# Optimization experiments

Hardware: AMD Instinct MI355X
Metric: run time of the kernel (lower is better)

Reference implementation:

```python
import jax, jax.numpy as jnp
import numpy as np

T, S, B, H, NH, F = 256, 128, 32, 1024, 16, 4096
D = H // NH  # head dim


def setup_inputs() -> dict:
    key = jax.random.key(0)
    ks = jax.random.split(key, 14)
    w = lambda k, shape: jax.random.normal(k, shape, jnp.float32) * 0.02
    return {
        "x": jax.random.normal(ks[0], (T, B, H), jnp.float32),
        "src_bias": jnp.zeros((B, 1, 1, S), jnp.float32),
        "tgt_bias": jnp.zeros((B, 1, 1, T), jnp.float32),
        "memory": jax.random.normal(ks[1], (S, B, H), jnp.float32),
        # cross-attention projections
        "Wq": w(ks[2], (H, H)), "bq": jnp.zeros((H,), jnp.float32),
        "Wk": w(ks[3], (H, H)), "bk": jnp.zeros((H,), jnp.float32),
        "Wv": w(ks[4], (H, H)), "bv": jnp.zeros((H,), jnp.float32),
        "Wo": w(ks[5], (H, H)), "bo": jnp.zeros((H,), jnp.float32),
        # feed-forward
        "W1": w(ks[6], (H, F)), "b1": jnp.zeros((F,), jnp.float32),
        "W2": w(ks[7], (F, H)), "b2": jnp.zeros((H,), jnp.float32),
        # LSTM gates: input = cat(ffn_x, attn_ctx, h) -> 3H, output 4H (i,j,f,o)
        "Wg": w(ks[8], (3 * H, 4 * H)), "bg": jnp.zeros((4 * H,), jnp.float32),
    }


def _cross_attention(xq, mem, bias, Wq, bq, Wk, bk, Wv, bv, Wo, bo):
    # xq: [B,T,H], mem: [B,S,H], bias: [B,1,1,S]
    b, t, h = xq.shape
    q = (xq @ Wq + bq).reshape(b, t, NH, D) * (D ** -0.5)
    k = (mem @ Wk + bk).reshape(b, -1, NH, D)
    v = (mem @ Wv + bv).reshape(b, -1, NH, D)
    logits = jnp.einsum("bqhd,bkhd->bhqk", q, k) + bias
    wts = jax.nn.softmax(logits, axis=-1)
    ctx = jnp.einsum("bhqk,bkhd->bqhd", wts, v).reshape(b, t, h)
    return ctx @ Wo + bo


def reference(x, src_bias, tgt_bias, memory, Wq, bq, Wk, bk, Wv, bv, Wo, bo,
              W1, b1, W2, b2, Wg, bg):
    # cross attention (time-major -> batch-major -> time-major)
    c_attn = _cross_attention(jnp.transpose(x, (1, 0, 2)),
                              jnp.transpose(memory, (1, 0, 2)),
                              src_bias, Wq, bq, Wk, bk, Wv, bv, Wo, bo)
    c_attn = jnp.transpose(c_attn, (1, 0, 2))  # [T,B,H]

    # feed-forward on x (dropout disabled / eval mode)
    ffn_x = jax.nn.relu(x @ W1 + b1) @ W2 + b2  # [T,B,H]

    xs = jnp.concatenate([ffn_x, c_attn], axis=-1)  # [T,B,2H]
    c0 = jnp.zeros((x.shape[1], H), x.dtype)
    h0 = jnp.zeros((x.shape[1], H), x.dtype)

    def step(carry, xt):
        c, h = carry
        g = jnp.concatenate([xt, h], axis=-1) @ Wg + bg  # [B,4H]
        i = jax.nn.sigmoid(g[:, :H])
        j = jnp.tanh(g[:, H:2 * H])
        f = jax.nn.sigmoid(g[:, 2 * H:3 * H])
        o = jax.nn.sigmoid(g[:, 3 * H:])
        new_c = f * c + i * j
        new_h = o * new_c  # THUMT LSTMCell default activation=None
        return (new_c, new_h), new_h

    (c_f, h_f), hiddens = jax.lax.scan(step, (c0, h0), xs)
    return hiddens, c_f, h_f
```

## Files before the change

### kernel.cpp

```cpp
#include <hip/hip_runtime.h>
#include <cstdint>
#include <cstddef>

#define T_  256
#define S_  128
#define B_  32
#define H_  1024
#define NH_ 16
#define D_  64
#define F_  4096
#define TB_ (T_*B_)
#define SB_ (S_*B_)

typedef unsigned short u16;
typedef unsigned int   u32;
typedef unsigned long long u64;
typedef __attribute__((ext_vector_type(8))) short s16x8;
typedef __attribute__((ext_vector_type(4))) float f32x4;
typedef __attribute__((ext_vector_type(4))) u32  u32x4;

static __device__ __forceinline__ float b2f(u16 u) {
  union { u32 i; float f; } cv; cv.i = ((u32)u) << 16; return cv.f;
}
static __device__ __forceinline__ u16 f2b(float f) {
  union { float f; u32 i; } cv; cv.f = f;
  u32 u = cv.i;
  u32 r = (u + 0x7fffu + ((u >> 16) & 1u)) >> 16;
  return (u16)r;
}
static __device__ __forceinline__ float sigm(float x) {
  return 1.0f / (1.0f + __expf(-x));
}
static __device__ __forceinline__ float tanh_fast(float x) {
  float e2 = __expf(2.0f * x);
  return 1.0f - 2.0f / (e2 + 1.0f);
}

typedef const __attribute__((address_space(1))) void* gvoidp;
typedef __attribute__((address_space(3))) void* lvoidp;
static __device__ __forceinline__ void gl_lds16(const void* g, void* l) {
  __builtin_amdgcn_global_load_lds((gvoidp)g, (lvoidp)l, 16, 0, 0);
}

static __device__ __forceinline__ void cast_task(const float* __restrict__ in,
                                                 u16* __restrict__ out, int lb, int tid) {
  int i = lb * 256 + tid;
  float4 v = reinterpret_cast<const float4*>(in)[i];
  ushort4 o;
  o.x = f2b(v.x); o.y = f2b(v.y); o.z = f2b(v.z); o.w = f2b(v.w);
  reinterpret_cast<ushort4*>(out)[i] = o;
}

static __device__ __forceinline__ void tr32(const float* __restrict__ in,
                                            u16* __restrict__ out,
                                            int R, int C, int lin, int tid,
                                            float tile[32][33]) {
  const int gx = C >> 5;
  const int bx = lin % gx, by = lin / gx;
  const int c0 = bx << 5, r0 = by << 5;
  const int tx = tid & 31, ty = tid >> 5;
  #pragma unroll
  for (int k = 0; k < 32; k += 8)
    tile[ty + k][tx] = in[(size_t)(r0 + ty + k) * C + c0 + tx];
  __syncthreads();
  #pragma unroll
  for (int k = 0; k < 32; k += 8)
    out[(size_t)(c0 + ty + k) * R + r0 + tx] = f2b(tile[tx][ty + k]);
}

#define NB_SENT 1
#define NB_CX   8192
#define NB_CM   4096
#define NB_TSQ  1024
#define NB_TW1  4096
#define NB_TW2  4096
#define NB_TGX  8192
#define NB_TWH  4096
#define NB_PREP (NB_SENT + NB_CX + NB_CM + 4*NB_TSQ + NB_TW1 + NB_TW2 + NB_TGX + NB_TWH)

__global__ __launch_bounds__(256) void prep_all(
    const float* __restrict__ x, const float* __restrict__ mem,
    const float* __restrict__ Wq, const float* __restrict__ Wk,
    const float* __restrict__ Wv, const float* __restrict__ Wo,
    const float* __restrict__ W1, const float* __restrict__ W2,
    const float* __restrict__ Wg,
    u16* __restrict__ xb, u16* __restrict__ memb,
    u16* __restrict__ WqT, u16* __restrict__ WkT, u16* __restrict__ WvT,
    u16* __restrict__ WoT, u16* __restrict__ W1T, u16* __restrict__ W2T,
    u16* __restrict__ WgxT, u16* __restrict__ WhT, u32* __restrict__ sent)
{
  __shared__ float tile[32][33];
  int b = blockIdx.x;
  const int tid = threadIdx.x;
  if (b < NB_SENT) { sent[tid] = 0; sent[tid + 256] = 0; return; }
  b -= NB_SENT;
  if (b < NB_CX) { cast_task(x, xb, b, tid); return; }      b -= NB_CX;
  if (b < NB_CM) { cast_task(mem, memb, b, tid); return; }  b -= NB_CM;
  if (b < NB_TSQ) { tr32(Wq, WqT, H_, H_, b, tid, tile); return; }  b -= NB_TSQ;
  if (b < NB_TSQ) { tr32(Wk, WkT, H_, H_, b, tid, tile); return; }  b -= NB_TSQ;
  if (b < NB_TSQ) { tr32(Wv, WvT, H_, H_, b, tid, tile); return; }  b -= NB_TSQ;
  if (b < NB_TSQ) { tr32(Wo, WoT, H_, H_, b, tid, tile); return; }  b -= NB_TSQ;
  if (b < NB_TW1) { tr32(W1, W1T, H_, F_, b, tid, tile); return; }  b -= NB_TW1;
  if (b < NB_TW2) { tr32(W2, W2T, F_, H_, b, tid, tile); return; }  b -= NB_TW2;
  if (b < NB_TGX) { tr32(Wg, WgxT, 2 * H_, 4 * H_, b, tid, tile); return; } b -= NB_TGX;
  tr32(Wg + (size_t)(2 * H_) * (4 * H_), WhT, H_, 4 * H_, b, tid, tile);
}

#define SBAR      asm volatile("s_barrier" ::: "memory")
#define VMCNT4    asm volatile("s_waitcnt vmcnt(4)" ::: "memory")
#define VMCNT0    asm volatile("s_waitcnt vmcnt(0)" ::: "memory")

struct GJob {
  const u16* A; const u16* Bt; u16* Out; const float* bias;
  int Kdim; int ostride; int relu; int gridx; int nblk; float scale;
};
struct GBatch { GJob j[4]; int starts[4]; int njobs; };

static __device__ __forceinline__ void stage_region(
    const u16* __restrict__ src, int Kdim, int row0,
    int kt, int kh, char* lds_region, int tid) {
  const int w  = tid >> 6;
  const int r  = tid >> 2;
  const int cs = (tid & 3) ^ ((tid >> 3) & 3);
  const int kbase = kt * 64 + kh * 32 + cs * 8;
  gl_lds16(src + (size_t)(row0 + r) * Kdim + kbase,        lds_region + w * 1024);
  gl_lds16(src + (size_t)(row0 + 128 + r) * Kdim + kbase,  lds_region + 8192 + w * 1024);
}

static __device__ __forceinline__ s16x8 ldsf(const char* sm, int base, int row, int quad) {
  return *(const s16x8*)(sm + base + row * 64 + ((quad ^ ((row >> 1) & 3)) << 4));
}

__global__ __launch_bounds__(512, 2) void gemm256(GBatch gb)
{
  __shared__ __align__(16) u16 smem[65536];
  char* sm = (char*)smem;
  const int bid = blockIdx.x;
  int ji = 0;
  #pragma unroll
  for (int t = 1; t < 4; t++)
    if (t < gb.njobs && bid >= gb.starts[t]) ji = t;
  const GJob J = gb.j[ji];
  const int lin = bid - gb.starts[ji];
  const int wg = (lin & 7) * (J.nblk >> 3) + (lin >> 3);
  const int bx = wg % J.gridx, by = wg / J.gridx;
  const int bm = by << 8, bn = bx << 8;

  const int tid = threadIdx.x;
  const int wavei = tid >> 6, lane = tid & 63;
  const int quad = lane >> 4, l16 = lane & 15;
  const int wm = wavei >> 2, wn = wavei & 3;
  const int NT = J.Kdim >> 6;
  const int arow = wm * 128;
  const int brow = wn * 64;

  f32x4 acc[8][4] = {};

  stage_region(J.A,  J.Kdim, bm, 0, 0, sm + 0,     tid);
  stage_region(J.Bt, J.Kdim, bn, 0, 0, sm + 32768, tid);
  stage_region(J.A,  J.Kdim, bm, 0, 1, sm + 16384, tid);
  stage_region(J.Bt, J.Kdim, bn, 0, 1, sm + 49152, tid);
  VMCNT4;
  SBAR;

  for (int kt = 0; kt < NT; kt++) {
    const int p = (kt & 1) << 16;
    const int q = p ^ 65536;
    const int Ab = p, Bb = p + 32768;
    const bool st = (kt + 1 < NT);
    s16x8 af[8], b0, b1;

    #pragma unroll
    for (int mi = 0; mi < 8; mi++)
      af[mi] = ldsf(sm, Ab, arow + mi * 16 + l16, quad);
    b0 = ldsf(sm, Bb, brow + l16, quad);
    b1 = ldsf(sm, Bb, brow + 16 + l16, quad);
    if (st) stage_region(J.A, J.Kdim, bm, kt + 1, 0, sm + q, tid);
    SBAR;
    __builtin_amdgcn_s_setprio(1);
    #pragma unroll
    for (int mi = 0; mi < 8; mi++) {
      acc[mi][0] = __builtin_amdgcn_mfma_f32_16x16x32_bf16(af[mi], b0, acc[mi][0], 0, 0, 0);
      acc[mi][1] = __builtin_amdgcn_mfma_f32_16x16x32_bf16(af[mi], b1, acc[mi][1], 0, 0, 0);
    }
    __builtin_amdgcn_s_setprio(0);
    SBAR;

    b0 = ldsf(sm, Bb, brow + 32 + l16, quad);
    b1 = ldsf(sm, Bb, brow + 48 + l16, quad);
    if (st) stage_region(J.Bt, J.Kdim, bn, kt + 1, 0, sm + q + 32768, tid);
    SBAR;
    __builtin_amdgcn_s_setprio(1);
    #pragma unroll
    for (int mi = 0; mi < 8; mi++) {
      acc[mi][2] = __builtin_amdgcn_mfma_f32_16x16x32_bf16(af[mi], b0, acc[mi][2], 0, 0, 0);
      acc[mi][3] = __builtin_amdgcn_mfma_f32_16x16x32_bf16(af[mi], b1, acc[mi][3], 0, 0, 0);
    }
    __builtin_amdgcn_s_setprio(0);
    if (st) { VMCNT4; } else { VMCNT0; }
    SBAR;

    const int Ab1 = Ab + 16384, Bb1 = Bb + 16384;
    #pragma unroll
    for (int mi = 0; mi < 8; mi++)
      af[mi] = ldsf(sm, Ab1, arow + mi * 16 + l16, quad);
    b0 = ldsf(sm, Bb1, brow + l16, quad);
    b1 = ldsf(sm, Bb1, brow + 16 + l16, quad);
    if (st) stage_region(J.A, J.Kdim, bm, kt + 1, 1, sm + q + 16384, tid);
    SBAR;
    __builtin_amdgcn_s_setprio(1);
    #pragma unroll
    for (int mi = 0; mi < 8; mi++) {
      acc[mi][0] = __builtin_amdgcn_mfma_f32_16x16x32_bf16(af[mi], b0, acc[mi][0], 0, 0, 0);
      acc[mi][1] = __builtin_amdgcn_mfma_f32_16x16x32_bf16(af[mi], b1, acc[mi][1], 0, 0, 0);
    }
    __builtin_amdgcn_s_setprio(0);
    SBAR;

    b0 = ldsf(sm, Bb1, brow + 32 + l16, quad);
    b1 = ldsf(sm, Bb1, brow + 48 + l16, quad);
    if (st) stage_region(J.Bt, J.Kdim, bn, kt + 1, 1, sm + q + 49152, tid);
    SBAR;
    __builtin_amdgcn_s_setprio(1);
    #pragma unroll
    for (int mi = 0; mi < 8; mi++) {
      acc[mi][2] = __builtin_amdgcn_mfma_f32_16x16x32_bf16(af[mi], b0, acc[mi][2], 0, 0, 0);
      acc[mi][3] = __builtin_amdgcn_mfma_f32_16x16x32_bf16(af[mi], b1, acc[mi][3], 0, 0, 0);
    }
    __builtin_amdgcn_s_setprio(0);
    if (st) { VMCNT4; }
    SBAR;
  }

  #pragma unroll
  for (int mi = 0; mi < 8; mi++) {
    #pragma unroll
    for (int nj = 0; nj < 4; nj++) {
      const int colo = bn + wn * 64 + nj * 16 + l16;
      const float bv = J.bias[colo];
      #pragma unroll
      for (int r = 0; r < 4; r++) {
        const int rowo = bm + wm * 128 + mi * 16 + quad * 4 + r;
        float vv = (acc[mi][nj][r] + bv) * J.scale;
        if (J.relu) vv = fmaxf(vv, 0.0f);
        J.Out[(size_t)rowo * J.ostride + colo] = f2b(vv);
      }
    }
  }
}

__global__ __launch_bounds__(256) void attn_kernel(
    const u16* __restrict__ q, const u16* __restrict__ k, const u16* __restrict__ v,
    const float* __restrict__ src_bias, u16* __restrict__ ctx)
{
  __shared__ u16 ks[S_ * D_];
  __shared__ u16 vs[S_ * D_];
  const int b  = blockIdx.x >> 4;
  const int nh = blockIdx.x & 15;
  const int tid = threadIdx.x;

  for (int i = tid; i < (S_ * D_) / 8; i += 256) {
    int s = i >> 3, c = (i & 7) * 8;
    *(uint4*)&ks[s * D_ + c] = *(const uint4*)&k[((size_t)(s * B_ + b)) * H_ + nh * D_ + c];
    *(uint4*)&vs[s * D_ + c] = *(const uint4*)&v[((size_t)(s * B_ + b)) * H_ + nh * D_ + c];
  }
  __syncthreads();

  const int t = tid;
  float qf[D_];
  const u16* qp = &q[((size_t)(t * B_ + b)) * H_ + nh * D_];
  #pragma unroll
  for (int c8 = 0; c8 < D_; c8 += 8) {
    uint4 qv = *(const uint4*)&qp[c8];
    const u16* pu = (const u16*)&qv;
    #pragma unroll
    for (int j = 0; j < 8; j++) qf[c8 + j] = b2f(pu[j]);
  }
  const float* bias = src_bias + b * S_;

  float m = -1e30f, l = 0.0f;
  for (int s = 0; s < S_; s++) {
    float dot = 0.0f;
    #pragma unroll
    for (int d = 0; d < D_; d++) dot += qf[d] * b2f(ks[s * D_ + d]);
    dot += bias[s];
    float nm = fmaxf(m, dot);
    l = l * __expf(m - nm) + __expf(dot - nm);
    m = nm;
  }
  float of[D_] = {};
  const float inv = 1.0f / l;
  for (int s = 0; s < S_; s++) {
    float dot = 0.0f;
    #pragma unroll
    for (int d = 0; d < D_; d++) dot += qf[d] * b2f(ks[s * D_ + d]);
    dot += bias[s];
    float w = __expf(dot - m) * inv;
    #pragma unroll
    for (int d = 0; d < D_; d++) of[d] += w * b2f(vs[s * D_ + d]);
  }
  u16* op = &ctx[((size_t)(t * B_ + b)) * H_ + nh * D_];
  #pragma unroll
  for (int c8 = 0; c8 < D_; c8 += 8) {
    u16 tmp[8];
    #pragma unroll
    for (int j = 0; j < 8; j++) tmp[j] = f2b(of[c8 + j]);
    *(uint4*)&op[c8] = *(const uint4*)tmp;
  }
}

#define ISSUE2(K) { \
  const u16* b0_ = hb + ((size_t)(wave * 16 + (K) * 2 + (quad >> 1))) * 512 + \
                   (quad & 1) * 8 + l16 * 16; \
  asm volatile("global_load_dwordx4 %0, %1, off sc0 sc1" : "=v"(ba[K][0]) : "v"(b0_) : "memory"); \
  asm volatile("global_load_dwordx4 %0, %1, off sc0 sc1" : "=v"(ba[K][1]) : "v"(b0_ + 256) : "memory"); }

#define DO_MFMA(A0,A1,KC)                                                           \
  { _Pragma("unroll") for (int g_ = 0; g_ < 3; g_++) {                              \
      s16x8 wf_ = *(const s16x8*)&Wl[wave][((g_ * 8 + (KC)) * 64 + lane) * 8];      \
      acc[g_][0] = __builtin_amdgcn_mfma_f32_16x16x32_bf16(A0, wf_, acc[g_][0], 0, 0, 0); \
      acc[g_][1] = __builtin_amdgcn_mfma_f32_16x16x32_bf16(A1, wf_, acc[g_][1], 0, 0, 0); } \
    acc[3][0] = __builtin_amdgcn_mfma_f32_16x16x32_bf16(A0, wo[KC], acc[3][0], 0, 0, 0);  \
    acc[3][1] = __builtin_amdgcn_mfma_f32_16x16x32_bf16(A1, wo[KC], acc[3][1], 0, 0, 0); }

#define CONSUME(K, NSTR) { \
  asm volatile("s_waitcnt vmcnt(" NSTR ")" ::: "memory"); \
  __builtin_amdgcn_sched_barrier(0); \
  DO_MFMA(ba[K][0], ba[K][1], K); }

__global__ __launch_bounds__(256, 1) void lstm_persistent(
    const u16* __restrict__ g_x, const u16* __restrict__ WhT,
    u16* __restrict__ hb16, u32* __restrict__ sent, float* __restrict__ out)
{
  __shared__ __align__(16) u16 Wl[4][3 * 8 * 64 * 8];
  __shared__ float P[4][4][32][17];
  const int bk = blockIdx.x, tid = threadIdx.x;
  const int wave = tid >> 6, lane = tid & 63;
  const int quad = lane >> 4, l16 = lane & 15;

  for (int i = lane; i < 3 * 8 * 64; i += 64) {
    const int g  = (i >> 9) & 3;
    const int kc = (i >> 6) & 7;
    const int row = g * H_ + bk * 16 + (lane & 15);
    const int col = wave * 256 + kc * 32 + (lane >> 4) * 8;
    *(uint4*)&Wl[wave][i * 8] = *(const uint4*)&WhT[(size_t)row * H_ + col];
  }
  s16x8 wo[8];
  {
    const int row = 3 * H_ + bk * 16 + (lane & 15);
    const int colb = wave * 256 + (lane >> 4) * 8;
    #pragma unroll
    for (int kc = 0; kc < 8; kc++)
      wo[kc] = *(const s16x8*)&WhT[(size_t)row * H_ + colb + kc * 32];
  }
  __syncthreads();

  const int pb = tid >> 4, pc = tid & 15;
  const int col = bk * 16 + pc;
  float creg[2] = {0.0f, 0.0f};

  float gxp[2][4];
  #pragma unroll
  for (int ii = 0; ii < 2; ii++)
    #pragma unroll
    for (int g = 0; g < 4; g++)
      gxp[ii][g] = b2f(g_x[((size_t)(pb + ii * 16)) * (4 * H_) + g * H_ + col]);

  s16x8 ba[8][2];

  for (int t = 0; t < T_; t++) {
    if (t > 0) {
      const u32 st = (u32)t;
      const u16* hb = hb16 + ((t & 1) ^ 1) * 32768;

      { const u32* sp = sent + ((size_t)(((t & 1) ^ 1) * 256 + wave * 64 + lane));
        u32 sv;
        do {
          asm volatile("global_load_dword %0, %1, off sc0 sc1\n\ts_waitcnt vmcnt(0)"
                       : "=v"(sv) : "v"(sp) : "memory");
        } while (!__all(sv == st)); }

      f32x4 acc[4][2] = {};
      ISSUE2(0) ISSUE2(1) ISSUE2(2) ISSUE2(3)
      ISSUE2(4) ISSUE2(5) ISSUE2(6) ISSUE2(7)
      CONSUME(0, "14") CONSUME(1, "12") CONSUME(2, "10") CONSUME(3, "8")
      CONSUME(4, "6")  CONSUME(5, "4")  CONSUME(6, "2")  CONSUME(7, "0")

      #pragma unroll
      for (int g = 0; g < 4; g++)
        #pragma unroll
        for (int mt = 0; mt < 2; mt++)
          #pragma unroll
          for (int r = 0; r < 4; r++)
            P[wave][g][mt * 16 + quad * 4 + r][l16] = acc[g][mt][r];
    }
    __syncthreads();

    float gs[2][4];
    #pragma unroll
    for (int ii = 0; ii < 2; ii++) {
      const int b_ = pb + ii * 16;
      #pragma unroll
      for (int g = 0; g < 4; g++) {
        float s = gxp[ii][g];
        if (t > 0) s += P[0][g][b_][pc] + P[1][g][b_][pc] + P[2][g][b_][pc] + P[3][g][b_][pc];
        gs[ii][g] = s;
      }
    }
    __syncthreads();

    float hn[2], cn[2];
    #pragma unroll
    for (int ii = 0; ii < 2; ii++) {
      const float iv = sigm(gs[ii][0]);
      const float jv = tanh_fast(gs[ii][1]);
      const float fv = sigm(gs[ii][2]);
      const float ov = sigm(gs[ii][3]);
      cn[ii] = fv * creg[ii] + iv * jv;
      hn[ii] = ov * cn[ii];
      creg[ii] = cn[ii];
    }

    {
      u32 lo0 = f2b(hn[0]), lo1 = f2b(hn[1]);
      u32 hi0 = __shfl_down(lo0, 1), hi1 = __shfl_down(lo1, 1);
      if ((pc & 1) == 0) {
        u32* hw32 = (u32*)(hb16 + (t & 1) * 32768);
        u32 dw0 = lo0 | (hi0 << 16);
        u32 dw1 = lo1 | (hi1 << 16);
        __hip_atomic_store(&hw32[(size_t)bk * 256 + pb * 8 + (pc >> 1)], dw0,
                           __ATOMIC_RELAXED, __HIP_MEMORY_SCOPE_AGENT);
        __hip_atomic_store(&hw32[(size_t)bk * 256 + (pb + 16) * 8 + (pc >> 1)], dw1,
                           __ATOMIC_RELAXED, __HIP_MEMORY_SCOPE_AGENT);
      }
      asm volatile("s_waitcnt vmcnt(0)" ::: "memory");
      if (lane == 0)
        __hip_atomic_store(&sent[(size_t)(t & 1) * 256 + bk * 4 + wave], (u32)(t + 1),
                           __ATOMIC_RELAXED, __HIP_MEMORY_SCOPE_AGENT);
    }

    #pragma unroll
    for (int ii = 0; ii < 2; ii++) {
      const int b_ = pb + ii * 16;
      out[(size_t)t * (B_ * H_) + b_ * H_ + col] = hn[ii];
      if (t == T_ - 1) {
        out[(size_t)T_ * B_ * H_ + b_ * H_ + col] = cn[ii];
        out[(size_t)T_ * B_ * H_ + B_ * H_ + b_ * H_ + col] = hn[ii];
      }
    }
    if (t < T_ - 1) {
      #pragma unroll
      for (int ii = 0; ii < 2; ii++)
        #pragma unroll
        for (int g = 0; g < 4; g++)
          gxp[ii][g] = b2f(g_x[((size_t)(t + 1) * B_ + pb + ii * 16) * (4 * H_) + g * H_ + col]);
    }
  }
}

extern "C" void kernel_launch(void* const* d_in, const int* in_sizes, int n_in,
                              void* d_out, int out_size, void* d_ws, size_t ws_size,
                              hipStream_t stream)
{
  const float* x        = (const float*)d_in[0];
  const float* src_bias = (const float*)d_in[1];
  const float* mem      = (const float*)d_in[3];
  const float* Wq = (const float*)d_in[4];  const float* bq = (const float*)d_in[5];
  const float* Wk = (const float*)d_in[6];  const float* bk = (const float*)d_in[7];
  const float* Wv = (const float*)d_in[8];  const float* bv = (const float*)d_in[9];
  const float* Wo = (const float*)d_in[10]; const float* bo = (const float*)d_in[11];
  const float* W1 = (const float*)d_in[12]; const float* b1f = (const float*)d_in[13];
  const float* W2 = (const float*)d_in[14]; const float* b2f_ = (const float*)d_in[15];
  const float* Wg = (const float*)d_in[16]; const float* bg = (const float*)d_in[17];
  float* out = (float*)d_out;

  char* p = (char*)d_ws;
  u16* xb   = (u16*)p; p += (size_t)TB_ * H_ * 2;
  u16* memb = (u16*)p; p += (size_t)SB_ * H_ * 2;
  u16* WqT  = (u16*)p; p += (size_t)H_ * H_ * 2;
  u16* WkT  = (u16*)p; p += (size_t)H_ * H_ * 2;
  u16* WvT  = (u16*)p; p += (size_t)H_ * H_ * 2;
  u16* WoT  = (u16*)p; p += (size_t)H_ * H_ * 2;
  u16* W1T  = (u16*)p; p += (size_t)F_ * H_ * 2;
  u16* W2T  = (u16*)p; p += (size_t)H_ * F_ * 2;
  u16* WgxT = (u16*)p; p += (size_t)(4 * H_) * (2 * H_) * 2;
  u16* WhT  = (u16*)p; p += (size_t)(4 * H_) * H_ * 2;
  u16* qb   = (u16*)p; p += (size_t)TB_ * H_ * 2;
  u16* kb   = (u16*)p; p += (size_t)SB_ * H_ * 2;
  u16* vb   = (u16*)p; p += (size_t)SB_ * H_ * 2;
  u16* ctxb = (u16*)p; p += (size_t)TB_ * H_ * 2;
  u16* xs   = (u16*)p; p += (size_t)TB_ * (2 * H_) * 2;
  u16* h1   = (u16*)p; p += (size_t)TB_ * F_ * 2;
  u16* hb16 = (u16*)p; p += (size_t)2 * 32768 * 2;
  u32* sent = (u32*)p; p += (size_t)2 * 256 * 4;
  u16* gx   = h1;

  prep_all<<<dim3(NB_PREP), dim3(256), 0, stream>>>(
      x, mem, Wq, Wk, Wv, Wo, W1, W2, Wg,
      xb, memb, WqT, WkT, WvT, WoT, W1T, W2T, WgxT, WhT, sent);

  GBatch gb1 = {};
  gb1.j[0] = { xb,   WqT, qb, bq,  H_, H_, 0, H_ / 256, (TB_ / 256) * (H_ / 256), 0.125f };
  gb1.j[1] = { memb, WkT, kb, bk,  H_, H_, 0, H_ / 256, (SB_ / 256) * (H_ / 256), 1.0f   };
  gb1.j[2] = { memb, WvT, vb, bv,  H_, H_, 0, H_ / 256, (SB_ / 256) * (H_ / 256), 1.0f   };
  gb1.j[3] = { xb,   W1T, h1, b1f, H_, F_, 1, F_ / 256, (TB_ / 256) * (F_ / 256), 1.0f   };
  gb1.starts[0] = 0;
  gb1.starts[1] = gb1.j[0].nblk;
  gb1.starts[2] = gb1.starts[1] + gb1.j[1].nblk;
  gb1.starts[3] = gb1.starts[2] + gb1.j[2].nblk;
  gb1.njobs = 4;
  const int nb1 = gb1.starts[3] + gb1.j[3].nblk;
  gemm256<<<dim3(nb1), dim3(512), 0, stream>>>(gb1);

  attn_kernel<<<dim3(B_ * NH_), dim3(256), 0, stream>>>(qb, kb, vb, src_bias, ctxb);

  GBatch gb2 = {};
  gb2.j[0] = { ctxb, WoT, xs + H_, bo,   H_, 2 * H_, 0, H_ / 256, (TB_ / 256) * (H_ / 256), 1.0f };
  gb2.j[1] = { h1,   W2T, xs,      b2f_, F_, 2 * H_, 0, H_ / 256, (TB_ / 256) * (H_ / 256), 1.0f };
  gb2.starts[0] = 0;
  gb2.starts[1] = gb2.j[0].nblk;
  gb2.njobs = 2;
  const int nb2 = gb2.starts[1] + gb2.j[1].nblk;
  gemm256<<<dim3(nb2), dim3(512), 0, stream>>>(gb2);

  GBatch gb3 = {};
  gb3.j[0] = { xs, WgxT, gx, bg, 2 * H_, 4 * H_, 0, 4 * H_ / 256, (TB_ / 256) * (4 * H_ / 256), 1.0f };
  gb3.starts[0] = 0;
  gb3.njobs = 1;
  gemm256<<<dim3(gb3.j[0].nblk), dim3(512), 0, stream>>>(gb3);

  lstm_persistent<<<dim3(64), dim3(256), 0, stream>>>(gx, WhT, hb16, sent, out);
}
```

Measured before the change: 1.591 ms.

## Embed step tags in LSTM hidden-state words to replace separate flag polling

The persistent LSTM kernel now stores each hidden value as a 32-bit word holding the step index in the high half and the bf16 value in the low half. Consumers load h directly, check the tags per k-chunk, and re-issue only the stale chunks while running MFMAs on the chunks that are already fresh. This removes the separate sentinel array, the producer's store-then-wait-then-flag sequence, and the consumer's spin on flags before loading. In exchange each h read moves twice as many bytes, adds per-element tag checks and packing, and leaves a retry loop that may spin on partial data.

```diff
diff --git a/kernel.cpp b/kernel.cpp
--- a/kernel.cpp
+++ b/kernel.cpp
@@ -42,6 +42,17 @@
   __builtin_amdgcn_global_load_lds((gvoidp)g, (lvoidp)l, 16, 0, 0);
 }
 
+static __device__ __forceinline__ bool fresh1(const u32x4 q, u32 st) {
+  return ((q[0] >> 16) == st) & ((q[1] >> 16) == st) &
+         ((q[2] >> 16) == st) & ((q[3] >> 16) == st);
+}
+static __device__ __forceinline__ s16x8 pack2(const u32x4 qa, const u32x4 qb) {
+  s16x8 r;
+  r[0] = (short)qa[0]; r[1] = (short)qa[1]; r[2] = (short)qa[2]; r[3] = (short)qa[3];
+  r[4] = (short)qb[0]; r[5] = (short)qb[1]; r[6] = (short)qb[2]; r[7] = (short)qb[3];
+  return r;
+}
+
 static __device__ __forceinline__ void cast_task(const float* __restrict__ in,
                                                  u16* __restrict__ out, int lb, int tid) {
   int i = lb * 256 + tid;
@@ -68,7 +79,7 @@
     out[(size_t)(c0 + ty + k) * R + r0 + tx] = f2b(tile[tx][ty + k]);
 }
 
-#define NB_SENT 1
+#define NB_ZERO 64
 #define NB_CX   8192
 #define NB_CM   4096
 #define NB_TSQ  1024
@@ -76,7 +87,7 @@
 #define NB_TW2  4096
 #define NB_TGX  8192
 #define NB_TWH  4096
-#define NB_PREP (NB_SENT + NB_CX + NB_CM + 4*NB_TSQ + NB_TW1 + NB_TW2 + NB_TGX + NB_TWH)
+#define NB_PREP (NB_ZERO + NB_CX + NB_CM + 4*NB_TSQ + NB_TW1 + NB_TW2 + NB_TGX + NB_TWH)
 
 __global__ __launch_bounds__(256) void prep_all(
     const float* __restrict__ x, const float* __restrict__ mem,
@@ -87,13 +98,16 @@
     u16* __restrict__ xb, u16* __restrict__ memb,
     u16* __restrict__ WqT, u16* __restrict__ WkT, u16* __restrict__ WvT,
     u16* __restrict__ WoT, u16* __restrict__ W1T, u16* __restrict__ W2T,
-    u16* __restrict__ WgxT, u16* __restrict__ WhT, u32* __restrict__ sent)
+    u16* __restrict__ WgxT, u16* __restrict__ WhT, u32* __restrict__ hseq)
 {
   __shared__ float tile[32][33];
   int b = blockIdx.x;
   const int tid = threadIdx.x;
-  if (b < NB_SENT) { sent[tid] = 0; sent[tid + 256] = 0; return; }
-  b -= NB_SENT;
+  if (b < NB_ZERO) {
+    *(u32x4*)&hseq[((size_t)b * 256 + tid) * 4] = (u32x4){0, 0, 0, 0};
+    return;
+  }
+  b -= NB_ZERO;
   if (b < NB_CX) { cast_task(x, xb, b, tid); return; }      b -= NB_CX;
   if (b < NB_CM) { cast_task(mem, memb, b, tid); return; }  b -= NB_CM;
   if (b < NB_TSQ) { tr32(Wq, WqT, H_, H_, b, tid, tile); return; }  b -= NB_TSQ;
@@ -309,28 +323,34 @@
   }
 }
 
-#define ISSUE2(K) { \
-  const u16* b0_ = hb + ((size_t)(wave * 16 + (K) * 2 + (quad >> 1))) * 512 + \
-                   (quad & 1) * 8 + l16 * 16; \
-  asm volatile("global_load_dwordx4 %0, %1, off sc0 sc1" : "=v"(ba[K][0]) : "v"(b0_) : "memory"); \
-  asm volatile("global_load_dwordx4 %0, %1, off sc0 sc1" : "=v"(ba[K][1]) : "v"(b0_ + 256) : "memory"); }
-
-#define DO_MFMA(A0,A1,KC)                                                           \
-  { _Pragma("unroll") for (int g_ = 0; g_ < 3; g_++) {                              \
-      s16x8 wf_ = *(const s16x8*)&Wl[wave][((g_ * 8 + (KC)) * 64 + lane) * 8];      \
-      acc[g_][0] = __builtin_amdgcn_mfma_f32_16x16x32_bf16(A0, wf_, acc[g_][0], 0, 0, 0); \
-      acc[g_][1] = __builtin_amdgcn_mfma_f32_16x16x32_bf16(A1, wf_, acc[g_][1], 0, 0, 0); } \
-    acc[3][0] = __builtin_amdgcn_mfma_f32_16x16x32_bf16(A0, wo[KC], acc[3][0], 0, 0, 0);  \
-    acc[3][1] = __builtin_amdgcn_mfma_f32_16x16x32_bf16(A1, wo[KC], acc[3][1], 0, 0, 0); }
-
-#define CONSUME(K, NSTR) { \
-  asm volatile("s_waitcnt vmcnt(" NSTR ")" ::: "memory"); \
-  __builtin_amdgcn_sched_barrier(0); \
-  DO_MFMA(ba[K][0], ba[K][1], K); }
+#define WAIT0 asm volatile("s_waitcnt vmcnt(0)" ::: "memory")
+
+#define ISSUE_K(BASE, K)  { \
+  const u32* bp_ = (BASE) + ((size_t)(wave * 16 + (K) * 2 + (quad >> 1))) * 512 + \
+                   (quad & 1) * 8; \
+  const u32* p0_ = bp_ + l16 * 16; \
+  const u32* p1_ = bp_ + (16 + l16) * 16; \
+  asm volatile("global_load_dwordx4 %0, %1, off sc0 sc1" : "=v"(bank[K][0]) : "v"(p0_) : "memory");     \
+  asm volatile("global_load_dwordx4 %0, %1, off sc0 sc1" : "=v"(bank[K][1]) : "v"(p0_ + 4) : "memory"); \
+  asm volatile("global_load_dwordx4 %0, %1, off sc0 sc1" : "=v"(bank[K][2]) : "v"(p1_) : "memory");     \
+  asm volatile("global_load_dwordx4 %0, %1, off sc0 sc1" : "=v"(bank[K][3]) : "v"(p1_ + 4) : "memory"); }
+
+#define FRESH_K(K) (fresh1(bank[K][0], st) & fresh1(bank[K][1], st) & \
+                    fresh1(bank[K][2], st) & fresh1(bank[K][3], st))
+
+#define MFMA_K(K) { \
+  s16x8 a0_ = pack2(bank[K][0], bank[K][1]); \
+  s16x8 a1_ = pack2(bank[K][2], bank[K][3]); \
+  _Pragma("unroll") for (int g_ = 0; g_ < 3; g_++) { \
+    s16x8 wf_ = *(const s16x8*)&Wl[wave][((g_ * 8 + (K)) * 64 + lane) * 8]; \
+    acc[g_][0] = __builtin_amdgcn_mfma_f32_16x16x32_bf16(a0_, wf_, acc[g_][0], 0, 0, 0); \
+    acc[g_][1] = __builtin_amdgcn_mfma_f32_16x16x32_bf16(a1_, wf_, acc[g_][1], 0, 0, 0); } \
+  acc[3][0] = __builtin_amdgcn_mfma_f32_16x16x32_bf16(a0_, wo[K], acc[3][0], 0, 0, 0); \
+  acc[3][1] = __builtin_amdgcn_mfma_f32_16x16x32_bf16(a1_, wo[K], acc[3][1], 0, 0, 0); }
 
 __global__ __launch_bounds__(256, 1) void lstm_persistent(
     const u16* __restrict__ g_x, const u16* __restrict__ WhT,
-    u16* __restrict__ hb16, u32* __restrict__ sent, float* __restrict__ out)
+    u32* __restrict__ hseq, float* __restrict__ out)
 {
   __shared__ __align__(16) u16 Wl[4][3 * 8 * 64 * 8];
   __shared__ float P[4][4][32][17];
@@ -366,25 +386,46 @@
     for (int g = 0; g < 4; g++)
       gxp[ii][g] = b2f(g_x[((size_t)(pb + ii * 16)) * (4 * H_) + g * H_ + col]);
 
-  s16x8 ba[8][2];
+  u32x4 bank[8][4];
 
   for (int t = 0; t < T_; t++) {
     if (t > 0) {
       const u32 st = (u32)t;
-      const u16* hb = hb16 + ((t & 1) ^ 1) * 32768;
-
-      { const u32* sp = sent + ((size_t)(((t & 1) ^ 1) * 256 + wave * 64 + lane));
-        u32 sv;
-        do {
-          asm volatile("global_load_dword %0, %1, off sc0 sc1\n\ts_waitcnt vmcnt(0)"
-                       : "=v"(sv) : "v"(sp) : "memory");
-        } while (!__all(sv == st)); }
-
+      const u32* hr = hseq + ((t & 1) ^ 1) * 32768;
       f32x4 acc[4][2] = {};
-      ISSUE2(0) ISSUE2(1) ISSUE2(2) ISSUE2(3)
-      ISSUE2(4) ISSUE2(5) ISSUE2(6) ISSUE2(7)
-      CONSUME(0, "14") CONSUME(1, "12") CONSUME(2, "10") CONSUME(3, "8")
-      CONSUME(4, "6")  CONSUME(5, "4")  CONSUME(6, "2")  CONSUME(7, "0")
+
+      ISSUE_K(hr, 0) ISSUE_K(hr, 1) ISSUE_K(hr, 2) ISSUE_K(hr, 3)
+      ISSUE_K(hr, 4) ISSUE_K(hr, 5) ISSUE_K(hr, 6) ISSUE_K(hr, 7)
+      WAIT0;
+      u32 need = 0;
+      #pragma unroll
+      for (int k = 0; k < 8; k++)
+        if (!__all(FRESH_K(k))) need |= (1u << k);
+      if (need) {
+        #pragma unroll
+        for (int k = 0; k < 8; k++)
+          if (need & (1u << k)) ISSUE_K(hr, k);
+      }
+      #pragma unroll
+      for (int k = 0; k < 8; k++)
+        if (!(need & (1u << k))) MFMA_K(k);
+      while (need) {
+        WAIT0;
+        u32 got = 0;
+        #pragma unroll
+        for (int k = 0; k < 8; k++)
+          if ((need & (1u << k)) && __all(FRESH_K(k))) got |= (1u << k);
+        const u32 rem = need & ~got;
+        if (rem) {
+          #pragma unroll
+          for (int k = 0; k < 8; k++)
+            if (rem & (1u << k)) ISSUE_K(hr, k);
+        }
+        #pragma unroll
+        for (int k = 0; k < 8; k++)
+          if (got & (1u << k)) MFMA_K(k);
+        need = rem;
+      }
 
       #pragma unroll
       for (int g = 0; g < 4; g++)
@@ -409,9 +450,11 @@
     }
     __syncthreads();
 
+    u32* hw = hseq + (t & 1) * 32768;
     float hn[2], cn[2];
     #pragma unroll
     for (int ii = 0; ii < 2; ii++) {
+      const int b_ = pb + ii * 16;
       const float iv = sigm(gs[ii][0]);
       const float jv = tanh_fast(gs[ii][1]);
       const float fv = sigm(gs[ii][2]);
@@ -419,24 +462,9 @@
       cn[ii] = fv * creg[ii] + iv * jv;
       hn[ii] = ov * cn[ii];
       creg[ii] = cn[ii];
-    }
-
-    {
-      u32 lo0 = f2b(hn[0]), lo1 = f2b(hn[1]);
-      u32 hi0 = __shfl_down(lo0, 1), hi1 = __shfl_down(lo1, 1);
-      if ((pc & 1) == 0) {
-        u32* hw32 = (u32*)(hb16 + (t & 1) * 32768);
-        u32 dw0 = lo0 | (hi0 << 16);
-        u32 dw1 = lo1 | (hi1 << 16);
-        __hip_atomic_store(&hw32[(size_t)bk * 256 + pb * 8 + (pc >> 1)], dw0,
-                           __ATOMIC_RELAXED, __HIP_MEMORY_SCOPE_AGENT);
-        __hip_atomic_store(&hw32[(size_t)bk * 256 + (pb + 16) * 8 + (pc >> 1)], dw1,
-                           __ATOMIC_RELAXED, __HIP_MEMORY_SCOPE_AGENT);
-      }
-      asm volatile("s_waitcnt vmcnt(0)" ::: "memory");
-      if (lane == 0)
-        __hip_atomic_store(&sent[(size_t)(t & 1) * 256 + bk * 4 + wave], (u32)(t + 1),
-                           __ATOMIC_RELAXED, __HIP_MEMORY_SCOPE_AGENT);
+      u32 dw = ((u32)(t + 1) << 16) | (u32)f2b(hn[ii]);
+      __hip_atomic_store(&hw[(size_t)bk * 512 + b_ * 16 + pc], dw,
+                         __ATOMIC_RELAXED, __HIP_MEMORY_SCOPE_AGENT);
     }
 
     #pragma unroll
@@ -491,13 +519,12 @@
   u16* ctxb = (u16*)p; p += (size_t)TB_ * H_ * 2;
   u16* xs   = (u16*)p; p += (size_t)TB_ * (2 * H_) * 2;
   u16* h1   = (u16*)p; p += (size_t)TB_ * F_ * 2;
-  u16* hb16 = (u16*)p; p += (size_t)2 * 32768 * 2;
-  u32* sent = (u32*)p; p += (size_t)2 * 256 * 4;
+  u32* hseq = (u32*)p; p += (size_t)2 * 32768 * 4;
   u16* gx   = h1;
 
   prep_all<<<dim3(NB_PREP), dim3(256), 0, stream>>>(
       x, mem, Wq, Wk, Wv, Wo, W1, W2, Wg,
-      xb, memb, WqT, WkT, WvT, WoT, W1T, W2T, WgxT, WhT, sent);
+      xb, memb, WqT, WkT, WvT, WoT, W1T, W2T, WgxT, WhT, hseq);
 
   GBatch gb1 = {};
   gb1.j[0] = { xb,   WqT, qb, bq,  H_, H_, 0, H_ / 256, (TB_ / 256) * (H_ / 256), 0.125f };
@@ -529,5 +556,5 @@
   gb3.njobs = 1;
   gemm256<<<dim3(gb3.j[0].nblk), dim3(512), 0, stream>>>(gb3);
 
-  lstm_persistent<<<dim3(64), dim3(256), 0, stream>>>(gx, WhT, hb16, sent, out);
-}
+  lstm_persistent<<<dim3(64), dim3(256), 0, stream>>>(gx, WhT, hseq, out);
+}
```

Result: slower. 2.763 ms (+73.7%).

## Fold attention output projection into LSTM gate weights algebraically

Applied to the files above, without the earlier changes.

Precomputes Wo·Wg_mid as a weight-only GEMM, run alongside the QKV/FFN1 batch, and folds bo·Wg_mid into the gate bias. The attention kernel then writes its context straight into the concatenated input buffer, so the per-token Wo projection over all T*B rows disappears from the second GEMM launch. In exchange it adds a 4096x1024x1024 GEMM on weights, a small bias-reduction pass in prep, and an extra bf16 rounding of the fused weight product, which may shift numerics slightly.

```diff
diff --git a/kernel.cpp b/kernel.cpp
--- a/kernel.cpp
+++ b/kernel.cpp
@@ -53,7 +53,7 @@
 
 static __device__ __forceinline__ void tr32(const float* __restrict__ in,
                                             u16* __restrict__ out,
-                                            int R, int C, int lin, int tid,
+                                            int R, int C, int ldo, int lin, int tid,
                                             float tile[32][33]) {
   const int gx = C >> 5;
   const int bx = lin % gx, by = lin / gx;
@@ -65,45 +65,66 @@
   __syncthreads();
   #pragma unroll
   for (int k = 0; k < 32; k += 8)
-    out[(size_t)(c0 + ty + k) * R + r0 + tx] = f2b(tile[tx][ty + k]);
-}
-
-#define NB_SENT 1
+    out[(size_t)(c0 + ty + k) * ldo + r0 + tx] = f2b(tile[tx][ty + k]);
+}
+
+#define NB_SZ   1
+#define NB_BG2  16
 #define NB_CX   8192
 #define NB_CM   4096
+#define NB_CWO  1024
 #define NB_TSQ  1024
 #define NB_TW1  4096
 #define NB_TW2  4096
-#define NB_TGX  8192
+#define NB_TGT  4096
+#define NB_TGB  4096
 #define NB_TWH  4096
-#define NB_PREP (NB_SENT + NB_CX + NB_CM + 4*NB_TSQ + NB_TW1 + NB_TW2 + NB_TGX + NB_TWH)
+#define NB_PREP (NB_SZ + NB_BG2 + NB_CX + NB_CM + NB_CWO + 3*NB_TSQ + NB_TW1 + NB_TW2 + NB_TGT + NB_TGB + NB_TWH)
 
 __global__ __launch_bounds__(256) void prep_all(
     const float* __restrict__ x, const float* __restrict__ mem,
     const float* __restrict__ Wq, const float* __restrict__ Wk,
     const float* __restrict__ Wv, const float* __restrict__ Wo,
     const float* __restrict__ W1, const float* __restrict__ W2,
-    const float* __restrict__ Wg,
+    const float* __restrict__ Wg, const float* __restrict__ bo,
+    const float* __restrict__ bg,
     u16* __restrict__ xb, u16* __restrict__ memb,
     u16* __restrict__ WqT, u16* __restrict__ WkT, u16* __restrict__ WvT,
-    u16* __restrict__ WoT, u16* __restrict__ W1T, u16* __restrict__ W2T,
-    u16* __restrict__ WgxT, u16* __restrict__ WhT, u32* __restrict__ sent)
+    u16* __restrict__ Wob, u16* __restrict__ W1T, u16* __restrict__ W2T,
+    u16* __restrict__ WgxT, u16* __restrict__ WgbT, u16* __restrict__ WhT,
+    u32* __restrict__ sent, float* __restrict__ zeros, float* __restrict__ bg2)
 {
   __shared__ float tile[32][33];
   int b = blockIdx.x;
   const int tid = threadIdx.x;
-  if (b < NB_SENT) { sent[tid] = 0; sent[tid + 256] = 0; return; }
-  b -= NB_SENT;
+  if (b < NB_SZ) {
+    sent[tid] = 0; sent[tid + 256] = 0;
+    float4 z = {0.f, 0.f, 0.f, 0.f};
+    ((float4*)zeros)[tid] = z;
+    return;
+  }
+  b -= NB_SZ;
+  if (b < NB_BG2) {
+    const int n = b * 256 + tid;
+    float a = bg[n];
+    #pragma unroll 8
+    for (int j = 0; j < H_; j++)
+      a += bo[j] * Wg[(size_t)(H_ + j) * (4 * H_) + n];
+    bg2[n] = a;
+    return;
+  }
+  b -= NB_BG2;
   if (b < NB_CX) { cast_task(x, xb, b, tid); return; }      b -= NB_CX;
   if (b < NB_CM) { cast_task(mem, memb, b, tid); return; }  b -= NB_CM;
-  if (b < NB_TSQ) { tr32(Wq, WqT, H_, H_, b, tid, tile); return; }  b -= NB_TSQ;
-  if (b < NB_TSQ) { tr32(Wk, WkT, H_, H_, b, tid, tile); return; }  b -= NB_TSQ;
-  if (b < NB_TSQ) { tr32(Wv, WvT, H_, H_, b, tid, tile); return; }  b -= NB_TSQ;
-  if (b < NB_TSQ) { tr32(Wo, WoT, H_, H_, b, tid, tile); return; }  b -= NB_TSQ;
-  if (b < NB_TW1) { tr32(W1, W1T, H_, F_, b, tid, tile); return; }  b -= NB_TW1;
-  if (b < NB_TW2) { tr32(W2, W2T, F_, H_, b, tid, tile); return; }  b -= NB_TW2;
-  if (b < NB_TGX) { tr32(Wg, WgxT, 2 * H_, 4 * H_, b, tid, tile); return; } b -= NB_TGX;
-  tr32(Wg + (size_t)(2 * H_) * (4 * H_), WhT, H_, 4 * H_, b, tid, tile);
+  if (b < NB_CWO) { cast_task(Wo, Wob, b, tid); return; }   b -= NB_CWO;
+  if (b < NB_TSQ) { tr32(Wq, WqT, H_, H_, H_, b, tid, tile); return; }  b -= NB_TSQ;
+  if (b < NB_TSQ) { tr32(Wk, WkT, H_, H_, H_, b, tid, tile); return; }  b -= NB_TSQ;
+  if (b < NB_TSQ) { tr32(Wv, WvT, H_, H_, H_, b, tid, tile); return; }  b -= NB_TSQ;
+  if (b < NB_TW1) { tr32(W1, W1T, H_, F_, H_, b, tid, tile); return; }  b -= NB_TW1;
+  if (b < NB_TW2) { tr32(W2, W2T, F_, H_, F_, b, tid, tile); return; }  b -= NB_TW2;
+  if (b < NB_TGT) { tr32(Wg, WgxT, H_, 4 * H_, 2 * H_, b, tid, tile); return; } b -= NB_TGT;
+  if (b < NB_TGB) { tr32(Wg + (size_t)H_ * (4 * H_), WgbT, H_, 4 * H_, H_, b, tid, tile); return; } b -= NB_TGB;
+  tr32(Wg + (size_t)(2 * H_) * (4 * H_), WhT, H_, 4 * H_, H_, b, tid, tile);
 }
 
 #define SBAR      asm volatile("s_barrier" ::: "memory")
@@ -114,7 +135,7 @@
   const u16* A; const u16* Bt; u16* Out; const float* bias;
   int Kdim; int ostride; int relu; int gridx; int nblk; float scale;
 };
-struct GBatch { GJob j[4]; int starts[4]; int njobs; };
+struct GBatch { GJob j[5]; int starts[5]; int njobs; };
 
 static __device__ __forceinline__ void stage_region(
     const u16* __restrict__ src, int Kdim, int row0,
@@ -138,7 +159,7 @@
   const int bid = blockIdx.x;
   int ji = 0;
   #pragma unroll
-  for (int t = 1; t < 4; t++)
+  for (int t = 1; t < 5; t++)
     if (t < gb.njobs && bid >= gb.starts[t]) ji = t;
   const GJob J = gb.j[ji];
   const int lin = bid - gb.starts[ji];
@@ -299,7 +320,7 @@
     #pragma unroll
     for (int d = 0; d < D_; d++) of[d] += w * b2f(vs[s * D_ + d]);
   }
-  u16* op = &ctx[((size_t)(t * B_ + b)) * H_ + nh * D_];
+  u16* op = &ctx[((size_t)(t * B_ + b)) * (2 * H_) + nh * D_];
   #pragma unroll
   for (int c8 = 0; c8 < D_; c8 += 8) {
     u16 tmp[8];
@@ -480,51 +501,53 @@
   u16* WqT  = (u16*)p; p += (size_t)H_ * H_ * 2;
   u16* WkT  = (u16*)p; p += (size_t)H_ * H_ * 2;
   u16* WvT  = (u16*)p; p += (size_t)H_ * H_ * 2;
-  u16* WoT  = (u16*)p; p += (size_t)H_ * H_ * 2;
+  u16* Wob  = (u16*)p; p += (size_t)H_ * H_ * 2;
   u16* W1T  = (u16*)p; p += (size_t)F_ * H_ * 2;
   u16* W2T  = (u16*)p; p += (size_t)H_ * F_ * 2;
   u16* WgxT = (u16*)p; p += (size_t)(4 * H_) * (2 * H_) * 2;
+  u16* WgbT = (u16*)p; p += (size_t)(4 * H_) * H_ * 2;
   u16* WhT  = (u16*)p; p += (size_t)(4 * H_) * H_ * 2;
   u16* qb   = (u16*)p; p += (size_t)TB_ * H_ * 2;
   u16* kb   = (u16*)p; p += (size_t)SB_ * H_ * 2;
   u16* vb   = (u16*)p; p += (size_t)SB_ * H_ * 2;
-  u16* ctxb = (u16*)p; p += (size_t)TB_ * H_ * 2;
   u16* xs   = (u16*)p; p += (size_t)TB_ * (2 * H_) * 2;
   u16* h1   = (u16*)p; p += (size_t)TB_ * F_ * 2;
   u16* hb16 = (u16*)p; p += (size_t)2 * 32768 * 2;
   u32* sent = (u32*)p; p += (size_t)2 * 256 * 4;
+  float* zeros = (float*)p; p += (size_t)1024 * 4;
+  float* bg2   = (float*)p; p += (size_t)(4 * H_) * 4;
   u16* gx   = h1;
 
   prep_all<<<dim3(NB_PREP), dim3(256), 0, stream>>>(
-      x, mem, Wq, Wk, Wv, Wo, W1, W2, Wg,
-      xb, memb, WqT, WkT, WvT, WoT, W1T, W2T, WgxT, WhT, sent);
+      x, mem, Wq, Wk, Wv, Wo, W1, W2, Wg, bo, bg,
+      xb, memb, WqT, WkT, WvT, Wob, W1T, W2T, WgxT, WgbT, WhT,
+      sent, zeros, bg2);
 
   GBatch gb1 = {};
-  gb1.j[0] = { xb,   WqT, qb, bq,  H_, H_, 0, H_ / 256, (TB_ / 256) * (H_ / 256), 0.125f };
-  gb1.j[1] = { memb, WkT, kb, bk,  H_, H_, 0, H_ / 256, (SB_ / 256) * (H_ / 256), 1.0f   };
-  gb1.j[2] = { memb, WvT, vb, bv,  H_, H_, 0, H_ / 256, (SB_ / 256) * (H_ / 256), 1.0f   };
-  gb1.j[3] = { xb,   W1T, h1, b1f, H_, F_, 1, F_ / 256, (TB_ / 256) * (F_ / 256), 1.0f   };
+  gb1.j[0] = { xb,   WqT,  qb,           bq,    H_, H_,     0, H_ / 256, (TB_ / 256) * (H_ / 256), 0.125f };
+  gb1.j[1] = { memb, WkT,  kb,           bk,    H_, H_,     0, H_ / 256, (SB_ / 256) * (H_ / 256), 1.0f   };
+  gb1.j[2] = { memb, WvT,  vb,           bv,    H_, H_,     0, H_ / 256, (SB_ / 256) * (H_ / 256), 1.0f   };
+  gb1.j[3] = { xb,   W1T,  h1,           b1f,   H_, F_,     1, F_ / 256, (TB_ / 256) * (F_ / 256), 1.0f   };
+  gb1.j[4] = { WgbT, Wob,  WgxT + H_,    zeros, H_, 2 * H_, 0, H_ / 256, (4 * H_ / 256) * (H_ / 256), 1.0f };
   gb1.starts[0] = 0;
   gb1.starts[1] = gb1.j[0].nblk;
   gb1.starts[2] = gb1.starts[1] + gb1.j[1].nblk;
   gb1.starts[3] = gb1.starts[2] + gb1.j[2].nblk;
-  gb1.njobs = 4;
-  const int nb1 = gb1.starts[3] + gb1.j[3].nblk;
+  gb1.starts[4] = gb1.starts[3] + gb1.j[3].nblk;
+  gb1.njobs = 5;
+  const int nb1 = gb1.starts[4] + gb1.j[4].nblk;
   gemm256<<<dim3(nb1), dim3(512), 0, stream>>>(gb1);
 
-  attn_kernel<<<dim3(B_ * NH_), dim3(256), 0, stream>>>(qb, kb, vb, src_bias, ctxb);
+  attn_kernel<<<dim3(B_ * NH_), dim3(256), 0, stream>>>(qb, kb, vb, src_bias, xs + H_);
 
   GBatch gb2 = {};
-  gb2.j[0] = { ctxb, WoT, xs + H_, bo,   H_, 2 * H_, 0, H_ / 256, (TB_ / 256) * (H_ / 256), 1.0f };
-  gb2.j[1] = { h1,   W2T, xs,      b2f_, F_, 2 * H_, 0, H_ / 256, (TB_ / 256) * (H_ / 256), 1.0f };
+  gb2.j[0] = { h1, W2T, xs, b2f_, F_, 2 * H_, 0, H_ / 256, (TB_ / 256) * (H_ / 256), 1.0f };
   gb2.starts[0] = 0;
-  gb2.starts[1] = gb2.j[0].nblk;
-  gb2.njobs = 2;
-  const int nb2 = gb2.starts[1] + gb2.j[1].nblk;
-  gemm256<<<dim3(nb2), dim3(512), 0, stream>>>(gb2);
+  gb2.njobs = 1;
+  gemm256<<<dim3(gb2.j[0].nblk), dim3(512), 0, stream>>>(gb2);
 
   GBatch gb3 = {};
-  gb3.j[0] = { xs, WgxT, gx, bg, 2 * H_, 4 * H_, 0, 4 * H_ / 256, (TB_ / 256) * (4 * H_ / 256), 1.0f };
+  gb3.j[0] = { xs, WgxT, gx, bg2, 2 * H_, 4 * H_, 0, 4 * H_ / 256, (TB_ / 256) * (4 * H_ / 256), 1.0f };
   gb3.starts[0] = 0;
   gb3.njobs = 1;
   gemm256<<<dim3(gb3.j[0].nblk), dim3(512), 0, stream>>>(gb3);
```

Result: slower. 1.658 ms (+4.2%).
